# Kernel tuning notes

Measured on AMD Instinct MI355X. Metric: run time of the kernel, lower is better.

## Reference

```python
import jax, jax.numpy as jnp
import numpy as np

B, L, C, N, TN = 1, 256, 128, 4, 4
CH = N * C  # 512, flattened hidden for routing projections
EPS = 1.1920929e-07  # torch.finfo(float32).eps (RMSNorm default eps)
LN_EPS = 1e-5
N_SINKHORN = 20  # training-mode iteration count


def sinkhorn_knopp(raw, n_iters):
    # raw: [..., n, n] real-valued logits -> doubly-stochastic matrix
    M = jnp.exp(raw)
    for _ in range(n_iters):
        M = M / jnp.sum(M, axis=-1, keepdims=True)  # row normalize
        M = M / jnp.sum(M, axis=-2, keepdims=True)  # col normalize
    return M


def setup_inputs() -> dict:
    key = jax.random.key(0)
    ks = jax.random.split(key, 8)
    s = 0.02
    eye = jnp.eye(N, dtype=jnp.float32)
    b_res = 2.0 * eye + (-2.0) * (1.0 - eye)
    return {
        "p": jax.random.normal(ks[0], (B, L, L, C), jnp.float32),
        "p_mask": jnp.ones((B, L, L), jnp.float32),
        "W_pre": jax.random.normal(ks[1], (N, CH), jnp.float32) * s,
        "W_post": jax.random.normal(ks[2], (N, CH), jnp.float32) * s,
        "W_res": jax.random.normal(ks[3], (N * N, CH), jnp.float32) * s,
        "b_pre": jnp.zeros((1, N), jnp.float32),
        "b_post": jnp.zeros((1, N), jnp.float32),
        "b_res": b_res,
        "alpha_pre": jnp.asarray(0.01, jnp.float32),
        "alpha_post": jnp.asarray(0.01, jnp.float32),
        "alpha_res": jnp.asarray(0.01, jnp.float32),
        "ln_g": jnp.ones((C,), jnp.float32),
        "ln_b": jnp.zeros((C,), jnp.float32),
        "W1": jax.random.normal(ks[4], (TN * C, C), jnp.float32) * s,
        "b1": jnp.zeros((TN * C,), jnp.float32),
        "W2": jax.random.normal(ks[5], (C, TN * C), jnp.float32) * s,
        "b2": jnp.zeros((C,), jnp.float32),
    }


def reference(p, p_mask, W_pre, W_post, W_res, b_pre, b_post, b_res,
              alpha_pre, alpha_post, alpha_res, ln_g, ln_b, W1, b1, W2, b2):
    # expand_input: [B,L,L,C] -> [B,L,L,n,C]
    x = jnp.broadcast_to(p[..., None, :], (B, L, L, N, C))
    # --- compute_mappings ---
    xf = x.reshape(B, L, L, CH)
    xn = xf * jax.lax.rsqrt(jnp.mean(xf * xf, axis=-1, keepdims=True) + EPS)
    H_pre_dyn = jnp.tanh(xn @ W_pre.T)                      # [B,L,L,n]
    H_post_dyn = jnp.tanh(xn @ W_post.T)                    # [B,L,L,n]
    H_res_dyn = jnp.tanh(xn @ W_res.T).reshape(B, L, L, N, N)
    H_pre = jax.nn.sigmoid(alpha_pre * H_pre_dyn + b_pre)   # [B,L,L,n]
    H_post = 2.0 * jax.nn.sigmoid(alpha_post * H_post_dyn + b_post)
    H_res = sinkhorn_knopp(alpha_res * H_res_dyn + b_res, N_SINKHORN)  # [B,L,L,n,n]
    # contract: H_pre [B,L,L,1,n] @ x [B,L,L,n,C] -> [B,L,L,C]
    p_c = jnp.einsum('blkn,blknc->blkc', H_pre, x)
    # --- PairTransition (LN -> Linear -> ReLU -> Linear, masked) ---
    mu = jnp.mean(p_c, axis=-1, keepdims=True)
    var = jnp.mean(jnp.square(p_c - mu), axis=-1, keepdims=True)
    m = (p_c - mu) * jax.lax.rsqrt(var + LN_EPS) * ln_g + ln_b
    h = jax.nn.relu(m @ W1.T + b1)                          # [B,L,L,TN*C]
    p_t = (h @ W2.T + b2) * p_mask[..., None]
    p_updated = p_c + p_t
    # expand back: H_post^T [B,L,L,n,1] * p_updated [B,L,L,1,C]
    p_expanded = H_post[..., :, None] * p_updated[..., None, :]
    # residual mixing: [B,L,L,n,n] @ [B,L,L,n,C]
    p_residual = jnp.einsum('blkmn,blknc->blkmc', H_res, x)
    return p_residual + p_expanded  # [B,L,L,n,C]
```

## Files before the change

### kernel.cpp

```cpp
#include <hip/hip_runtime.h>
#include <stdint.h>

#define LLTOT 65536
#define CDIM  128
#define TPIX  32

typedef float f32x4 __attribute__((ext_vector_type(4)));
typedef short s16x8 __attribute__((ext_vector_type(8)));

#define MFMA16(a, b, c) __builtin_amdgcn_mfma_f32_16x16x32_bf16((a), (b), (c), 0, 0, 0)

__device__ __align__(16) unsigned short g_wefff[2 * 4 * 64 * 8];
__device__ __align__(16) unsigned short g_w1gf[32 * 4 * 64 * 8];
__device__ __align__(16) unsigned short g_w2f [8 * 16 * 64 * 8];
__device__ __align__(16) float  g_hA[512];
__device__ __align__(16) float  g_w1gs[512];
__device__ __align__(16) float  g_A[LLTOT * 4];
__device__ __align__(16) float  g_B[LLTOT * 4];
__device__ __align__(16) float2 g_simi[LLTOT];
__device__ __align__(16) unsigned short g_pbf[LLTOT * CDIM];

__device__ __forceinline__ unsigned short f2bf(float f) {
    union { float f; uint32_t u; } v; v.f = f;
    uint32_t u = v.u;
    return (unsigned short)((u + 0x7FFFu + ((u >> 16) & 1u)) >> 16);
}
__device__ __forceinline__ uint32_t pack2(float a, float b) {
    return (uint32_t)f2bf(a) | ((uint32_t)f2bf(b) << 16);
}
__device__ __forceinline__ float bf2f(uint32_t lo16) { return __uint_as_float(lo16 << 16); }

__device__ __forceinline__ float fast_tanh(float x) {
    float cx = fminf(fmaxf(x, -10.f), 10.f);
    float e = __expf(2.f * cx);
    return (e - 1.f) * __builtin_amdgcn_rcpf(e + 1.f);
}
__device__ __forceinline__ float fast_sig(float z) {
    return __builtin_amdgcn_rcpf(1.f + __expf(-z));
}

__global__ void prep_kernel(const float* __restrict__ Wpre, const float* __restrict__ Wpost,
                            const float* __restrict__ Wres, const float* __restrict__ W1,
                            const float* __restrict__ W2, const float* __restrict__ ln_g,
                            const float* __restrict__ ln_b, const float* __restrict__ b1) {
    int b = blockIdx.x, t = threadIdx.x;
    if (b == 264) {
        int j = t;
        float sg = 0.f, sb = 0.f;
        const float* row = W1 + j * 128;
        #pragma unroll 4
        for (int c = 0; c < 128; c += 4) {
            float4 wv = *(const float4*)(row + c);
            float4 gv = *(const float4*)(ln_g + c);
            float4 bv = *(const float4*)(ln_b + c);
            sg += wv.x*gv.x + wv.y*gv.y + wv.z*gv.z + wv.w*gv.w;
            sb += wv.x*bv.x + wv.y*bv.y + wv.z*bv.z + wv.w*bv.w;
        }
        g_hA[j]   = b1[j] + sb;
        g_w1gs[j] = sg;
        return;
    }
    int idx = b * 512 + t;
    if (idx < 4096) {
        int e = idx & 7, lane = (idx >> 3) & 63, kk = (idx >> 9) & 3, tile = idx >> 11;
        int o = tile * 16 + (lane & 15);
        int c = kk * 32 + (lane >> 4) * 8 + e;
        float v = 0.f;
        if (o < 4)        v = Wpre[o*512+c] + Wpre[o*512+128+c] + Wpre[o*512+256+c] + Wpre[o*512+384+c];
        else if (o < 8)   { int j = o - 4;  v = Wpost[j*512+c] + Wpost[j*512+128+c] + Wpost[j*512+256+c] + Wpost[j*512+384+c]; }
        else if (o < 24)  { int j = o - 8;  v = Wres[j*512+c] + Wres[j*512+128+c] + Wres[j*512+256+c] + Wres[j*512+384+c]; }
        g_wefff[idx] = f2bf(v);
    } else if (idx < 69632) {
        int d = idx - 4096;
        int e = d & 7, lane = (d >> 3) & 63, kk = (d >> 9) & 3, jt = d >> 11;
        int j = jt * 16 + (lane & 15);
        int c = kk * 32 + (lane >> 4) * 8 + e;
        g_w1gf[d] = f2bf(W1[j * 128 + c] * ln_g[c]);
    } else if (idx < 135168) {
        int d = idx - 69632;
        int e = d & 7, lane = (d >> 3) & 63, kk = (d >> 9) & 15, ct = d >> 13;
        int c = ct * 16 + (lane & 15);
        int k = kk * 32 + (lane >> 4) * 8 + e;
        g_w2f[d] = f2bf(W2[c * 512 + k]);
    }
}

__global__ void __launch_bounds__(256, 4) route_kernel(
    const float* __restrict__ p, const float* __restrict__ p_mask,
    const float* __restrict__ b_pre, const float* __restrict__ b_post, const float* __restrict__ b_res,
    const float* __restrict__ a_pre, const float* __restrict__ a_post, const float* __restrict__ a_res)
{
    const int l = threadIdx.x & 63;
    const int gw = (int)((blockIdx.x * 256 + threadIdx.x) >> 6);
    const int g = l >> 4, pixl = l & 15;
    const size_t gpix = (size_t)gw * 16 + pixl;

    float s = 0.f, ss = 0.f;
    s16x8 pf[4];
    const float* prow = p + gpix * 128 + g * 8;
    #pragma unroll
    for (int kk = 0; kk < 4; ++kk) {
        float4 va = *(const float4*)(prow + kk * 32);
        float4 vb = *(const float4*)(prow + kk * 32 + 4);
        s  += va.x + va.y + va.z + va.w + vb.x + vb.y + vb.z + vb.w;
        ss += va.x*va.x + va.y*va.y + va.z*va.z + va.w*va.w
            + vb.x*vb.x + vb.y*vb.y + vb.z*vb.z + vb.w*vb.w;
        s16x8 f;
        f[0] = (short)f2bf(va.x); f[1] = (short)f2bf(va.y);
        f[2] = (short)f2bf(va.z); f[3] = (short)f2bf(va.w);
        f[4] = (short)f2bf(vb.x); f[5] = (short)f2bf(vb.y);
        f[6] = (short)f2bf(vb.z); f[7] = (short)f2bf(vb.w);
        pf[kk] = f;
        *(s16x8*)(g_pbf + ((size_t)(gw * 4 + kk) * 64 + l) * 8) = f;
    }
    s  += __shfl_xor(s, 16);  ss += __shfl_xor(ss, 16);
    s  += __shfl_xor(s, 32);  ss += __shfl_xor(ss, 32);
    float mu = s * (1.f / 128.f), mq = ss * (1.f / 128.f);
    float rv  = rsqrtf(mq + 1.1920929e-07f);
    float var = mq - mu * mu;

    f32x4 y1 = {0.f, 0.f, 0.f, 0.f}, y2 = {0.f, 0.f, 0.f, 0.f};
    #pragma unroll
    for (int kk = 0; kk < 4; ++kk) {
        s16x8 a0 = *(const s16x8*)(g_wefff + ((size_t)(kk) * 64 + l) * 8);
        s16x8 a1 = *(const s16x8*)(g_wefff + ((size_t)(4 + kk) * 64 + l) * 8);
        y1 = MFMA16(a0, pf[kk], y1);
        y2 = MFMA16(a1, pf[kk], y2);
    }
    #pragma unroll
    for (int r = 0; r < 4; ++r) { y1[r] *= rv; y2[r] *= rv; }

    float apre = a_pre[0], apost = a_post[0], ares = a_res[0];

    float sp_loc = 0.f;
    #pragma unroll
    for (int r = 0; r < 4; ++r)
        sp_loc += fast_sig(apre * fast_tanh(y1[r]) + b_pre[r]);
    float sp = __shfl(sp_loc, pixl);

    float hp0 = 2.f * fast_sig(apost * fast_tanh(y1[0]) + b_post[0]);
    float hp1 = 2.f * fast_sig(apost * fast_tanh(y1[1]) + b_post[1]);
    float hp2 = 2.f * fast_sig(apost * fast_tanh(y1[2]) + b_post[2]);
    float hp3 = 2.f * fast_sig(apost * fast_tanh(y1[3]) + b_post[3]);

    int m = (g + 2) & 3;
    bool lo = g < 2;
    float M0 = __expf(ares * fast_tanh(lo ? y2[0] : y1[0]) + b_res[m * 4 + 0]);
    float M1 = __expf(ares * fast_tanh(lo ? y2[1] : y1[1]) + b_res[m * 4 + 1]);
    float M2 = __expf(ares * fast_tanh(lo ? y2[2] : y1[2]) + b_res[m * 4 + 2]);
    float M3 = __expf(ares * fast_tanh(lo ? y2[3] : y1[3]) + b_res[m * 4 + 3]);
    #pragma unroll 1
    for (int it = 0; it < 20; ++it) {
        float ri = __builtin_amdgcn_rcpf(M0 + M1 + M2 + M3);
        M0 *= ri; M1 *= ri; M2 *= ri; M3 *= ri;
        float c0 = M0, c1 = M1, c2 = M2, c3 = M3;
        c0 += __shfl_xor(c0, 16); c1 += __shfl_xor(c1, 16); c2 += __shfl_xor(c2, 16); c3 += __shfl_xor(c3, 16);
        c0 += __shfl_xor(c0, 32); c1 += __shfl_xor(c1, 32); c2 += __shfl_xor(c2, 32); c3 += __shfl_xor(c3, 32);
        M0 *= __builtin_amdgcn_rcpf(c0); M1 *= __builtin_amdgcn_rcpf(c1);
        M2 *= __builtin_amdgcn_rcpf(c2); M3 *= __builtin_amdgcn_rcpf(c3);
    }
    float rm = M0 + M1 + M2 + M3;

    float h0b = __shfl(hp0, pixl + 16);
    float h1b = __shfl(hp1, pixl + 16);
    float h2b = __shfl(hp2, pixl + 16);
    float h3b = __shfl(hp3, pixl + 16);
    float hpm = (m & 2) ? ((m & 1) ? h3b : h2b) : ((m & 1) ? h1b : h0b);

    float msk = p_mask[gpix];
    g_A[gpix * 4 + m] = rm + hpm * sp;
    g_B[gpix * 4 + m] = hpm * msk;
    if (l < 16) {
        float istd = rsqrtf(sp * sp * var + 1e-5f);
        g_simi[gpix] = make_float2(sp * istd, sp * mu * istd);
    }
}

__global__ void __launch_bounds__(512, 4) mlp_kernel(const float* __restrict__ b2g,
                                                     float* __restrict__ out)
{
    __shared__ __align__(16) unsigned short h_s[TPIX * 512];

    const int t = threadIdx.x;
    const int w = t >> 6, l = t & 63, lr = l & 15, lk = l >> 4;
    const int blk = blockIdx.x;
    const size_t base = (size_t)blk * 32;

    s16x8 pf[2][4];
    #pragma unroll
    for (int it = 0; it < 2; ++it)
        #pragma unroll
        for (int kk = 0; kk < 4; ++kk)
            pf[it][kk] = *(const s16x8*)(g_pbf + ((size_t)((blk * 2 + it) * 4 + kk) * 64 + l) * 8);

    float2 sim0 = g_simi[base + lr];
    float2 sim1 = g_simi[base + 16 + lr];

    f32x4 acc1[4][2] = {};
    #pragma unroll
    for (int kk = 0; kk < 4; ++kk)
        #pragma unroll
        for (int jt = 0; jt < 4; ++jt) {
            s16x8 a = *(const s16x8*)(g_w1gf + ((size_t)((w * 4 + jt) * 4 + kk) * 64 + l) * 8);
            acc1[jt][0] = MFMA16(a, pf[0][kk], acc1[jt][0]);
            acc1[jt][1] = MFMA16(a, pf[1][kk], acc1[jt][1]);
        }

    #pragma unroll
    for (int jt = 0; jt < 4; ++jt) {
        int j0 = w * 64 + jt * 16 + lk * 4;
        float4 wg = *(const float4*)(g_w1gs + j0);
        float4 ha = *(const float4*)(g_hA + j0);
        #pragma unroll
        for (int it = 0; it < 2; ++it) {
            int i = it * 16 + lr;
            float si = it ? sim1.x : sim0.x;
            float mi = it ? sim1.y : sim0.y;
            f32x4 v = acc1[jt][it];
            float h0 = fmaxf(fmaf(si, v[0], fmaf(-mi, wg.x, ha.x)), 0.f);
            float h1 = fmaxf(fmaf(si, v[1], fmaf(-mi, wg.y, ha.y)), 0.f);
            float h2 = fmaxf(fmaf(si, v[2], fmaf(-mi, wg.z, ha.z)), 0.f);
            float h3 = fmaxf(fmaf(si, v[3], fmaf(-mi, wg.w, ha.w)), 0.f);
            uint2 uu;
            uu.x = pack2(h0, h1);
            uu.y = pack2(h2, h3);
            uint32_t off = (uint32_t)(i * 1024 + j0 * 2) ^ ((i & 7) << 5);
            *(uint2*)((char*)h_s + off) = uu;
        }
    }
    __syncthreads();

    f32x4 acc2[2] = {};
    #pragma unroll 4
    for (int kk = 0; kk < 16; ++kk) {
        s16x8 a = *(const s16x8*)(g_w2f + ((size_t)(w * 16 + kk) * 64 + l) * 8);
        s16x8 b0, b1;
        {
            uint32_t off = (uint32_t)(lr * 1024 + kk * 64 + lk * 16) ^ ((lr & 7) << 5);
            b0 = *(const s16x8*)((const char*)h_s + off);
        }
        {
            int i = 16 + lr;
            uint32_t off = (uint32_t)(i * 1024 + kk * 64 + lk * 16) ^ ((i & 7) << 5);
            b1 = *(const s16x8*)((const char*)h_s + off);
        }
        acc2[0] = MFMA16(a, b0, acc2[0]);
        acc2[1] = MFMA16(a, b1, acc2[1]);
    }

    const int c0 = w * 16 + lk * 4;
    float4 b2v = *(const float4*)(b2g + c0);
    #pragma unroll
    for (int it = 0; it < 2; ++it) {
        int i = it * 16 + lr;
        f32x4 Av = *(const f32x4*)(g_A + (base + i) * 4);
        f32x4 Bv = *(const f32x4*)(g_B + (base + i) * 4);
        uint2 pb = *(const uint2*)(g_pbf
                     + ((size_t)((blk * 2 + it) * 4 + (w >> 1)) * 64
                        + ((w & 1) * 2 + (lk >> 1)) * 16 + lr) * 8
                     + (lk & 1) * 4);
        float p0 = bf2f(pb.x & 0xffffu), p1 = __uint_as_float(pb.x & 0xffff0000u);
        float p2 = bf2f(pb.y & 0xffffu), p3 = __uint_as_float(pb.y & 0xffff0000u);
        float d0 = acc2[it][0] + b2v.x, d1 = acc2[it][1] + b2v.y;
        float d2 = acc2[it][2] + b2v.z, d3 = acc2[it][3] + b2v.w;
        float* og = out + (base + i) * 512 + c0;
        #pragma unroll
        for (int m = 0; m < 4; ++m) {
            f32x4 o;
            o[0] = Av[m] * p0 + Bv[m] * d0;
            o[1] = Av[m] * p1 + Bv[m] * d1;
            o[2] = Av[m] * p2 + Bv[m] * d2;
            o[3] = Av[m] * p3 + Bv[m] * d3;
            *(f32x4*)(og + m * 128) = o;
        }
    }
}

extern "C" void kernel_launch(void* const* d_in, const int* in_sizes, int n_in,
                              void* d_out, int out_size, void* d_ws, size_t ws_size,
                              hipStream_t stream) {
    const float* p      = (const float*)d_in[0];
    const float* p_mask = (const float*)d_in[1];
    const float* W_pre  = (const float*)d_in[2];
    const float* W_post = (const float*)d_in[3];
    const float* W_res  = (const float*)d_in[4];
    const float* b_pre  = (const float*)d_in[5];
    const float* b_post = (const float*)d_in[6];
    const float* b_res  = (const float*)d_in[7];
    const float* a_pre  = (const float*)d_in[8];
    const float* a_post = (const float*)d_in[9];
    const float* a_res  = (const float*)d_in[10];
    const float* ln_g   = (const float*)d_in[11];
    const float* ln_b   = (const float*)d_in[12];
    const float* W1     = (const float*)d_in[13];
    const float* b1     = (const float*)d_in[14];
    const float* W2     = (const float*)d_in[15];
    const float* b2     = (const float*)d_in[16];
    float* out = (float*)d_out;

    prep_kernel<<<265, 512, 0, stream>>>(W_pre, W_post, W_res, W1, W2, ln_g, ln_b, b1);
    route_kernel<<<1024, 256, 0, stream>>>(p, p_mask, b_pre, b_post, b_res,
                                           a_pre, a_post, a_res);
    mlp_kernel<<<2048, 512, 0, stream>>>(b2, out);
}
```

Measured before the change: 78.06 us.

## Fuse routing and MLP kernels, passing intermediates through shared memory

Merges the route and MLP kernels into one launch. Two waves per block compute the routing coefficients and the bf16 copy of p for that block's 32 pixels and write them to LDS. All eight waves then run the MLP from LDS instead of reading global scratch buffers. This removes one launch and the global write/read round trip of the bf16 p copy and the A/B/simi arrays. In exchange, six of the eight waves sit idle during the serial routing phase (including the 20-iteration Sinkhorn loop), and LDS use per block rises.

```diff
diff --git a/kernel.cpp b/kernel.cpp
--- a/kernel.cpp
+++ b/kernel.cpp
@@ -15,10 +15,6 @@
 __device__ __align__(16) unsigned short g_w2f [8 * 16 * 64 * 8];
 __device__ __align__(16) float  g_hA[512];
 __device__ __align__(16) float  g_w1gs[512];
-__device__ __align__(16) float  g_A[LLTOT * 4];
-__device__ __align__(16) float  g_B[LLTOT * 4];
-__device__ __align__(16) float2 g_simi[LLTOT];
-__device__ __align__(16) unsigned short g_pbf[LLTOT * CDIM];
 
 __device__ __forceinline__ unsigned short f2bf(float f) {
     union { float f; uint32_t u; } v; v.f = f;
@@ -85,147 +81,145 @@
     }
 }
 
-__global__ void __launch_bounds__(256, 4) route_kernel(
+__global__ void __launch_bounds__(512, 4) fused_kernel(
     const float* __restrict__ p, const float* __restrict__ p_mask,
     const float* __restrict__ b_pre, const float* __restrict__ b_post, const float* __restrict__ b_res,
-    const float* __restrict__ a_pre, const float* __restrict__ a_post, const float* __restrict__ a_res)
+    const float* __restrict__ a_pre, const float* __restrict__ a_post, const float* __restrict__ a_res,
+    const float* __restrict__ b2g, float* __restrict__ out)
 {
-    const int l = threadIdx.x & 63;
-    const int gw = (int)((blockIdx.x * 256 + threadIdx.x) >> 6);
-    const int g = l >> 4, pixl = l & 15;
-    const size_t gpix = (size_t)gw * 16 + pixl;
-
-    float s = 0.f, ss = 0.f;
-    s16x8 pf[4];
-    const float* prow = p + gpix * 128 + g * 8;
+    __shared__ __align__(16) unsigned short pf_lds[8 * 64 * 8];
+    __shared__ __align__(16) unsigned short h_s[TPIX * 512];
+    __shared__ __align__(16) float A_s[TPIX * 4], B_s[TPIX * 4];
+    __shared__ __align__(16) float2 simi_s[TPIX];
+
+    const int t = threadIdx.x;
+    const int w = t >> 6, l = t & 63, lr = l & 15, lk = l >> 4;
+    const size_t base = (size_t)blockIdx.x * 32;
+
+    if (w < 2) {
+        const int g = lk, pixl = lr;
+        const size_t gpix = base + w * 16 + pixl;
+
+        float s = 0.f, ss = 0.f;
+        s16x8 pf[4];
+        const float* prow = p + gpix * 128 + g * 8;
+        #pragma unroll
+        for (int kk = 0; kk < 4; ++kk) {
+            float4 va = *(const float4*)(prow + kk * 32);
+            float4 vb = *(const float4*)(prow + kk * 32 + 4);
+            s  += va.x + va.y + va.z + va.w + vb.x + vb.y + vb.z + vb.w;
+            ss += va.x*va.x + va.y*va.y + va.z*va.z + va.w*va.w
+                + vb.x*vb.x + vb.y*vb.y + vb.z*vb.z + vb.w*vb.w;
+            s16x8 f;
+            f[0] = (short)f2bf(va.x); f[1] = (short)f2bf(va.y);
+            f[2] = (short)f2bf(va.z); f[3] = (short)f2bf(va.w);
+            f[4] = (short)f2bf(vb.x); f[5] = (short)f2bf(vb.y);
+            f[6] = (short)f2bf(vb.z); f[7] = (short)f2bf(vb.w);
+            pf[kk] = f;
+            *(s16x8*)(pf_lds + (size_t)(w * 4 + kk) * 512 + l * 8) = f;
+        }
+        s  += __shfl_xor(s, 16);  ss += __shfl_xor(ss, 16);
+        s  += __shfl_xor(s, 32);  ss += __shfl_xor(ss, 32);
+        float mu = s * (1.f / 128.f), mq = ss * (1.f / 128.f);
+        float rv  = rsqrtf(mq + 1.1920929e-07f);
+        float var = mq - mu * mu;
+
+        f32x4 y1 = {0.f, 0.f, 0.f, 0.f}, y2 = {0.f, 0.f, 0.f, 0.f};
+        #pragma unroll
+        for (int kk = 0; kk < 4; ++kk) {
+            s16x8 a0 = *(const s16x8*)(g_wefff + ((size_t)(kk) * 64 + l) * 8);
+            s16x8 a1 = *(const s16x8*)(g_wefff + ((size_t)(4 + kk) * 64 + l) * 8);
+            y1 = MFMA16(a0, pf[kk], y1);
+            y2 = MFMA16(a1, pf[kk], y2);
+        }
+        #pragma unroll
+        for (int r = 0; r < 4; ++r) { y1[r] *= rv; y2[r] *= rv; }
+
+        float apre = a_pre[0], apost = a_post[0], ares = a_res[0];
+
+        float sp_loc = 0.f;
+        #pragma unroll
+        for (int r = 0; r < 4; ++r)
+            sp_loc += fast_sig(apre * fast_tanh(y1[r]) + b_pre[r]);
+        float sp = __shfl(sp_loc, pixl);
+
+        float hp0 = 2.f * fast_sig(apost * fast_tanh(y1[0]) + b_post[0]);
+        float hp1 = 2.f * fast_sig(apost * fast_tanh(y1[1]) + b_post[1]);
+        float hp2 = 2.f * fast_sig(apost * fast_tanh(y1[2]) + b_post[2]);
+        float hp3 = 2.f * fast_sig(apost * fast_tanh(y1[3]) + b_post[3]);
+
+        int m = (g + 2) & 3;
+        bool lo = g < 2;
+        float M0 = __expf(ares * fast_tanh(lo ? y2[0] : y1[0]) + b_res[m * 4 + 0]);
+        float M1 = __expf(ares * fast_tanh(lo ? y2[1] : y1[1]) + b_res[m * 4 + 1]);
+        float M2 = __expf(ares * fast_tanh(lo ? y2[2] : y1[2]) + b_res[m * 4 + 2]);
+        float M3 = __expf(ares * fast_tanh(lo ? y2[3] : y1[3]) + b_res[m * 4 + 3]);
+        #pragma unroll 1
+        for (int it = 0; it < 20; ++it) {
+            float ri = __builtin_amdgcn_rcpf(M0 + M1 + M2 + M3);
+            M0 *= ri; M1 *= ri; M2 *= ri; M3 *= ri;
+            float c0 = M0, c1 = M1, c2 = M2, c3 = M3;
+            c0 += __shfl_xor(c0, 16); c1 += __shfl_xor(c1, 16); c2 += __shfl_xor(c2, 16); c3 += __shfl_xor(c3, 16);
+            c0 += __shfl_xor(c0, 32); c1 += __shfl_xor(c1, 32); c2 += __shfl_xor(c2, 32); c3 += __shfl_xor(c3, 32);
+            M0 *= __builtin_amdgcn_rcpf(c0); M1 *= __builtin_amdgcn_rcpf(c1);
+            M2 *= __builtin_amdgcn_rcpf(c2); M3 *= __builtin_amdgcn_rcpf(c3);
+        }
+        float rm = M0 + M1 + M2 + M3;
+
+        float h0b = __shfl(hp0, pixl + 16);
+        float h1b = __shfl(hp1, pixl + 16);
+        float h2b = __shfl(hp2, pixl + 16);
+        float h3b = __shfl(hp3, pixl + 16);
+        float hpm = (m & 2) ? ((m & 1) ? h3b : h2b) : ((m & 1) ? h1b : h0b);
+
+        float msk = p_mask[gpix];
+        int pix = w * 16 + pixl;
+        A_s[pix * 4 + m] = rm + hpm * sp;
+        B_s[pix * 4 + m] = hpm * msk;
+        if (l < 16) {
+            float istd = rsqrtf(sp * sp * var + 1e-5f);
+            simi_s[pix] = make_float2(sp * istd, sp * mu * istd);
+        }
+    }
+    __syncthreads();
+
+    f32x4 acc1[4][2] = {};
     #pragma unroll
     for (int kk = 0; kk < 4; ++kk) {
-        float4 va = *(const float4*)(prow + kk * 32);
-        float4 vb = *(const float4*)(prow + kk * 32 + 4);
-        s  += va.x + va.y + va.z + va.w + vb.x + vb.y + vb.z + vb.w;
-        ss += va.x*va.x + va.y*va.y + va.z*va.z + va.w*va.w
-            + vb.x*vb.x + vb.y*vb.y + vb.z*vb.z + vb.w*vb.w;
-        s16x8 f;
-        f[0] = (short)f2bf(va.x); f[1] = (short)f2bf(va.y);
-        f[2] = (short)f2bf(va.z); f[3] = (short)f2bf(va.w);
-        f[4] = (short)f2bf(vb.x); f[5] = (short)f2bf(vb.y);
-        f[6] = (short)f2bf(vb.z); f[7] = (short)f2bf(vb.w);
-        pf[kk] = f;
-        *(s16x8*)(g_pbf + ((size_t)(gw * 4 + kk) * 64 + l) * 8) = f;
-    }
-    s  += __shfl_xor(s, 16);  ss += __shfl_xor(ss, 16);
-    s  += __shfl_xor(s, 32);  ss += __shfl_xor(ss, 32);
-    float mu = s * (1.f / 128.f), mq = ss * (1.f / 128.f);
-    float rv  = rsqrtf(mq + 1.1920929e-07f);
-    float var = mq - mu * mu;
-
-    f32x4 y1 = {0.f, 0.f, 0.f, 0.f}, y2 = {0.f, 0.f, 0.f, 0.f};
-    #pragma unroll
-    for (int kk = 0; kk < 4; ++kk) {
-        s16x8 a0 = *(const s16x8*)(g_wefff + ((size_t)(kk) * 64 + l) * 8);
-        s16x8 a1 = *(const s16x8*)(g_wefff + ((size_t)(4 + kk) * 64 + l) * 8);
-        y1 = MFMA16(a0, pf[kk], y1);
-        y2 = MFMA16(a1, pf[kk], y2);
-    }
-    #pragma unroll
-    for (int r = 0; r < 4; ++r) { y1[r] *= rv; y2[r] *= rv; }
-
-    float apre = a_pre[0], apost = a_post[0], ares = a_res[0];
-
-    float sp_loc = 0.f;
-    #pragma unroll
-    for (int r = 0; r < 4; ++r)
-        sp_loc += fast_sig(apre * fast_tanh(y1[r]) + b_pre[r]);
-    float sp = __shfl(sp_loc, pixl);
-
-    float hp0 = 2.f * fast_sig(apost * fast_tanh(y1[0]) + b_post[0]);
-    float hp1 = 2.f * fast_sig(apost * fast_tanh(y1[1]) + b_post[1]);
-    float hp2 = 2.f * fast_sig(apost * fast_tanh(y1[2]) + b_post[2]);
-    float hp3 = 2.f * fast_sig(apost * fast_tanh(y1[3]) + b_post[3]);
-
-    int m = (g + 2) & 3;
-    bool lo = g < 2;
-    float M0 = __expf(ares * fast_tanh(lo ? y2[0] : y1[0]) + b_res[m * 4 + 0]);
-    float M1 = __expf(ares * fast_tanh(lo ? y2[1] : y1[1]) + b_res[m * 4 + 1]);
-    float M2 = __expf(ares * fast_tanh(lo ? y2[2] : y1[2]) + b_res[m * 4 + 2]);
-    float M3 = __expf(ares * fast_tanh(lo ? y2[3] : y1[3]) + b_res[m * 4 + 3]);
-    #pragma unroll 1
-    for (int it = 0; it < 20; ++it) {
-        float ri = __builtin_amdgcn_rcpf(M0 + M1 + M2 + M3);
-        M0 *= ri; M1 *= ri; M2 *= ri; M3 *= ri;
-        float c0 = M0, c1 = M1, c2 = M2, c3 = M3;
-        c0 += __shfl_xor(c0, 16); c1 += __shfl_xor(c1, 16); c2 += __shfl_xor(c2, 16); c3 += __shfl_xor(c3, 16);
-        c0 += __shfl_xor(c0, 32); c1 += __shfl_xor(c1, 32); c2 += __shfl_xor(c2, 32); c3 += __shfl_xor(c3, 32);
-        M0 *= __builtin_amdgcn_rcpf(c0); M1 *= __builtin_amdgcn_rcpf(c1);
-        M2 *= __builtin_amdgcn_rcpf(c2); M3 *= __builtin_amdgcn_rcpf(c3);
-    }
-    float rm = M0 + M1 + M2 + M3;
-
-    float h0b = __shfl(hp0, pixl + 16);
-    float h1b = __shfl(hp1, pixl + 16);
-    float h2b = __shfl(hp2, pixl + 16);
-    float h3b = __shfl(hp3, pixl + 16);
-    float hpm = (m & 2) ? ((m & 1) ? h3b : h2b) : ((m & 1) ? h1b : h0b);
-
-    float msk = p_mask[gpix];
-    g_A[gpix * 4 + m] = rm + hpm * sp;
-    g_B[gpix * 4 + m] = hpm * msk;
-    if (l < 16) {
-        float istd = rsqrtf(sp * sp * var + 1e-5f);
-        g_simi[gpix] = make_float2(sp * istd, sp * mu * istd);
-    }
-}
-
-__global__ void __launch_bounds__(512, 4) mlp_kernel(const float* __restrict__ b2g,
-                                                     float* __restrict__ out)
-{
-    __shared__ __align__(16) unsigned short h_s[TPIX * 512];
-
-    const int t = threadIdx.x;
-    const int w = t >> 6, l = t & 63, lr = l & 15, lk = l >> 4;
-    const int blk = blockIdx.x;
-    const size_t base = (size_t)blk * 32;
-
-    s16x8 pf[2][4];
-    #pragma unroll
-    for (int it = 0; it < 2; ++it)
-        #pragma unroll
-        for (int kk = 0; kk < 4; ++kk)
-            pf[it][kk] = *(const s16x8*)(g_pbf + ((size_t)((blk * 2 + it) * 4 + kk) * 64 + l) * 8);
-
-    float2 sim0 = g_simi[base + lr];
-    float2 sim1 = g_simi[base + 16 + lr];
-
-    f32x4 acc1[4][2] = {};
-    #pragma unroll
-    for (int kk = 0; kk < 4; ++kk)
+        s16x8 b0 = *(const s16x8*)(pf_lds + (size_t)(kk) * 512 + l * 8);
+        s16x8 b1 = *(const s16x8*)(pf_lds + (size_t)(4 + kk) * 512 + l * 8);
         #pragma unroll
         for (int jt = 0; jt < 4; ++jt) {
             s16x8 a = *(const s16x8*)(g_w1gf + ((size_t)((w * 4 + jt) * 4 + kk) * 64 + l) * 8);
-            acc1[jt][0] = MFMA16(a, pf[0][kk], acc1[jt][0]);
-            acc1[jt][1] = MFMA16(a, pf[1][kk], acc1[jt][1]);
-        }
-
-    #pragma unroll
-    for (int jt = 0; jt < 4; ++jt) {
-        int j0 = w * 64 + jt * 16 + lk * 4;
-        float4 wg = *(const float4*)(g_w1gs + j0);
-        float4 ha = *(const float4*)(g_hA + j0);
-        #pragma unroll
-        for (int it = 0; it < 2; ++it) {
-            int i = it * 16 + lr;
-            float si = it ? sim1.x : sim0.x;
-            float mi = it ? sim1.y : sim0.y;
-            f32x4 v = acc1[jt][it];
-            float h0 = fmaxf(fmaf(si, v[0], fmaf(-mi, wg.x, ha.x)), 0.f);
-            float h1 = fmaxf(fmaf(si, v[1], fmaf(-mi, wg.y, ha.y)), 0.f);
-            float h2 = fmaxf(fmaf(si, v[2], fmaf(-mi, wg.z, ha.z)), 0.f);
-            float h3 = fmaxf(fmaf(si, v[3], fmaf(-mi, wg.w, ha.w)), 0.f);
-            uint2 uu;
-            uu.x = pack2(h0, h1);
-            uu.y = pack2(h2, h3);
-            uint32_t off = (uint32_t)(i * 1024 + j0 * 2) ^ ((i & 7) << 5);
-            *(uint2*)((char*)h_s + off) = uu;
+            acc1[jt][0] = MFMA16(a, b0, acc1[jt][0]);
+            acc1[jt][1] = MFMA16(a, b1, acc1[jt][1]);
+        }
+    }
+
+    {
+        float2 sim0 = simi_s[lr];
+        float2 sim1 = simi_s[16 + lr];
+        #pragma unroll
+        for (int jt = 0; jt < 4; ++jt) {
+            int j0 = w * 64 + jt * 16 + lk * 4;
+            float4 wg = *(const float4*)(g_w1gs + j0);
+            float4 ha = *(const float4*)(g_hA + j0);
+            #pragma unroll
+            for (int it = 0; it < 2; ++it) {
+                int i = it * 16 + lr;
+                float si = it ? sim1.x : sim0.x;
+                float mi = it ? sim1.y : sim0.y;
+                f32x4 v = acc1[jt][it];
+                float h0 = fmaxf(fmaf(si, v[0], fmaf(-mi, wg.x, ha.x)), 0.f);
+                float h1 = fmaxf(fmaf(si, v[1], fmaf(-mi, wg.y, ha.y)), 0.f);
+                float h2 = fmaxf(fmaf(si, v[2], fmaf(-mi, wg.z, ha.z)), 0.f);
+                float h3 = fmaxf(fmaf(si, v[3], fmaf(-mi, wg.w, ha.w)), 0.f);
+                uint2 uu;
+                uu.x = pack2(h0, h1);
+                uu.y = pack2(h2, h3);
+                uint32_t off = (uint32_t)(i * 1024 + j0 * 2) ^ ((i & 7) << 5);
+                *(uint2*)((char*)h_s + off) = uu;
+            }
         }
     }
     __syncthreads();
@@ -253,12 +247,12 @@
     #pragma unroll
     for (int it = 0; it < 2; ++it) {
         int i = it * 16 + lr;
-        f32x4 Av = *(const f32x4*)(g_A + (base + i) * 4);
-        f32x4 Bv = *(const f32x4*)(g_B + (base + i) * 4);
-        uint2 pb = *(const uint2*)(g_pbf
-                     + ((size_t)((blk * 2 + it) * 4 + (w >> 1)) * 64
-                        + ((w & 1) * 2 + (lk >> 1)) * 16 + lr) * 8
-                     + (lk & 1) * 4);
+        f32x4 Av = *(const f32x4*)(A_s + i * 4);
+        f32x4 Bv = *(const f32x4*)(B_s + i * 4);
+        const unsigned short* pe = pf_lds
+            + ((size_t)(it * 4 + (w >> 1)) * 64 + ((w & 1) * 2 + (lk >> 1)) * 16 + lr) * 8
+            + (lk & 1) * 4;
+        uint2 pb = *(const uint2*)pe;
         float p0 = bf2f(pb.x & 0xffffu), p1 = __uint_as_float(pb.x & 0xffff0000u);
         float p2 = bf2f(pb.y & 0xffffu), p3 = __uint_as_float(pb.y & 0xffff0000u);
         float d0 = acc2[it][0] + b2v.x, d1 = acc2[it][1] + b2v.y;
@@ -299,7 +293,6 @@
     float* out = (float*)d_out;
 
     prep_kernel<<<265, 512, 0, stream>>>(W_pre, W_post, W_res, W1, W2, ln_g, ln_b, b1);
-    route_kernel<<<1024, 256, 0, stream>>>(p, p_mask, b_pre, b_post, b_res,
-                                           a_pre, a_post, a_res);
-    mlp_kernel<<<2048, 512, 0, stream>>>(b2, out);
-}
+    fused_kernel<<<2048, 512, 0, stream>>>(p, p_mask, b_pre, b_post, b_res,
+                                           a_pre, a_post, a_res, b2, out);
+}
```

Result: faster. 74.89 us (-4.1%).
